# Kernel tuning notes

Measured on AMD Instinct MI355X. Metric: run time of the kernel, lower is better.

The kernel has to match this reference:

```python
import jax, jax.numpy as jnp
import numpy as np

G_DIMS = [30, 30, 24, 18, 18]
G_DOWN = [10, 10, 8, 6, 6]
S_DIM = 10
N_OBJ = 45
N_STREAMS = 5
P_DIM = sum(G_DOWN) * S_DIM          # 400
HID = 20 * S_DIM                     # 200
FREQS = np.array([0.01, 0.7, 0.91, 0.97, 0.99], dtype=np.float32)
DECAY, N_ITERS = 0.8, 5
HEB_LR, HEB_FORGET = 0.5, 0.9999
LOGSIG_RATIO, LOGSIG_OFFSET = 6.0, -2.0
B, T = 256, 8
_G_OFFS = np.concatenate([[0], np.cumsum(G_DIMS)]).astype(int)


def _leaky_clamp(x):
    # f(clamp(x, -1, 1)) with f = leaky_relu (torch default slope 0.01)
    return jax.nn.leaky_relu(jnp.clip(x, -1.0, 1.0))


def _scale_log_sigma(raw, temp=1.0):
    return LOGSIG_OFFSET + temp * jnp.tanh(raw / LOGSIG_RATIO) * LOGSIG_RATIO


def _downsample(g):  # [B, 120] -> [B, 40]; take first g_down dims of each stream
    return jnp.concatenate([g[:, o:o + d] for o, d in zip(_G_OFFS[:-1], G_DOWN)], axis=1)


def setup_inputs() -> dict:
    key = jax.random.key(0)
    ks = jax.random.split(key, 10)
    return {
        "g_seq": jax.random.normal(ks[0], (B, T, sum(G_DIMS)), jnp.float32),
        "x_idx": jax.random.randint(ks[1], (B, T), 0, N_OBJ),
        "W_comp": jax.random.normal(ks[2], (N_OBJ, S_DIM), jnp.float32) * 0.3,
        "W_repeat": jax.random.normal(ks[3], (P_DIM, sum(G_DOWN)), jnp.float32) * 0.2,
        "W_tile": jax.random.normal(ks[4], (P_DIM, N_STREAMS * S_DIM), jnp.float32) * 0.2,
        "W_tile0": jax.random.normal(ks[5], (G_DOWN[0] * S_DIM, S_DIM), jnp.float32) * 0.2,
        "w_x": jnp.ones((), jnp.float32),
        "b_x": jnp.zeros((S_DIM,), jnp.float32),
        "W1": jax.random.normal(ks[6], (S_DIM, HID), jnp.float32) * 0.2,
        "b1": jnp.zeros((HID,), jnp.float32),
        "W2": jax.random.normal(ks[7], (HID, N_OBJ), jnp.float32) * 0.1,
        "b2": jnp.zeros((N_OBJ,), jnp.float32),
        "W_lv1": jax.random.normal(ks[8], (P_DIM, P_DIM), jnp.float32) * 0.05,
        "b_lv1": jnp.zeros((P_DIM,), jnp.float32),
        "W_lv2": jax.random.normal(ks[9], (P_DIM, P_DIM), jnp.float32) * 0.05,
        "b_lv2": jnp.zeros((P_DIM,), jnp.float32),
    }


def _forward(g_seq, x_onehot, W_comp, W_repeat, W_tile, W_tile0, w_x, b_x,
             W1, b1, W2, b2, W_lv1, b_lv1, W_lv2, b_lv2):
    Bn = g_seq.shape[0]
    freqs = jnp.asarray(FREQS, dtype=g_seq.dtype)

    def step(carry, xs):
        M, x_filt = carry            # M: [B,P,P] Hebbian memory; x_filt: [B,5,10]
        g_t, x_t = xs                # g_t: [B,120], x_t: [B,45]
        # sensory compression + per-stream exponential temporal filtering
        x_c = x_t @ W_comp                                          # [B,10]
        x_filt = (1.0 - freqs)[None, :, None] * x_filt + freqs[None, :, None] * x_c[:, None, :]
        x_flat = x_filt.reshape(Bn, N_STREAMS * S_DIM)              # [B,50]
        # fused p-vector formation (_scriptable_fused_form_p)
        g_down = _downsample(g_t)                                   # [B,40]
        g_exp = g_down @ W_repeat.T                                 # [B,400]
        x_exp = x_flat @ W_tile.T                                   # [B,400]
        p_inf = _leaky_clamp(g_exp * x_exp)
        # attractor retrieval seeded from g projected to p-space (_scriptable_transform_g_to_p)
        h = _leaky_clamp(g_exp)
        for _ in range(N_ITERS):                                    # memory_iterations
            h = _leaky_clamp(DECAY * h + jnp.einsum('bij,bj->bi', M, h))
        p_ret = h
        # precision-weighted Gaussian fusion of inference and memory estimates
        lv1 = _scale_log_sigma(p_inf @ W_lv1 + b_lv1)
        lv2 = _scale_log_sigma(p_ret @ W_lv2 + b_lv2)
        inv1, inv2 = jnp.exp(-lv1), jnp.exp(-lv2)
        var_c = 1.0 / (inv1 + inv2)
        p_t = var_c * (p_inf * inv1 + p_ret * inv2)
        # Hebbian update: M <- lambda*M + eta*(p - p_hat)(p + p_hat)^T
        M = HEB_FORGET * M + HEB_LR * jnp.einsum('bi,bj->bij', p_t - p_ret, p_t + p_ret)
        # generative decode from stream-0 slice of p (GenerativeNetwork.forward_decode)
        x_s = w_x * (p_t[:, :G_DOWN[0] * S_DIM] @ W_tile0) + b_x    # [B,10]
        logits = jax.nn.elu(x_s @ W1 + b1) @ W2 + b2                # [B,45]
        return (M, x_filt), logits

    M0 = jnp.zeros((Bn, P_DIM, P_DIM), g_seq.dtype)
    xf0 = jnp.zeros((Bn, N_STREAMS, S_DIM), g_seq.dtype)
    xs = (jnp.swapaxes(g_seq, 0, 1), jnp.swapaxes(x_onehot, 0, 1))
    _, logits = jax.lax.scan(step, (M0, xf0), xs)                   # [T,B,45]
    return jnp.swapaxes(logits, 0, 1)                               # [B,T,45]


def reference(g_seq, x_idx, W_comp, W_repeat, W_tile, W_tile0, w_x, b_x,
              W1, b1, W2, b2, W_lv1, b_lv1, W_lv2, b_lv2):
    x_onehot = jax.nn.one_hot(x_idx, N_OBJ, dtype=g_seq.dtype)
    return _forward(g_seq, x_onehot, W_comp, W_repeat, W_tile, W_tile0, w_x, b_x,
                    W1, b1, W2, b2, W_lv1, b_lv1, W_lv2, b_lv2)
```

## Files before the change

### kernel.cpp

```cpp
#include <hip/hip_runtime.h>

#define kT 8
#define kG 120
#define kP 400
#define kObj 45
#define kS 10
#define kHid 200
#define NL 12
#define NV 24
#define NC (NL + NV)

__device__ __constant__ int c_gmap[40] = {
    0,1,2,3,4,5,6,7,8,9,
    30,31,32,33,34,35,36,37,38,39,
    60,61,62,63,64,65,66,67,
    84,85,86,87,88,89,
    102,103,104,105,106,107};

__device__ __constant__ float c_freq[5] = {0.01f, 0.7f, 0.91f, 0.97f, 0.99f};

__device__ __forceinline__ float leaky_clamp(float x) {
    x = fminf(fmaxf(x, -1.0f), 1.0f);
    return x > 0.0f ? x : 0.01f * x;
}

__global__ __launch_bounds__(512, 1) void tem_kernel(
    const float* __restrict__ g_seq, const int* __restrict__ x_idx,
    const float* __restrict__ W_comp, const float* __restrict__ W_repeat,
    const float* __restrict__ W_tile, const float* __restrict__ W_tile0,
    const float* __restrict__ w_x, const float* __restrict__ b_x,
    const float* __restrict__ W1, const float* __restrict__ b1,
    const float* __restrict__ W2, const float* __restrict__ b2,
    const float* __restrict__ W_lv1, const float* __restrict__ b_lv1,
    const float* __restrict__ W_lv2, const float* __restrict__ b_lv2,
    float* __restrict__ out)
{
    const int b   = blockIdx.x;
    const int tid = threadIdx.x;
    const int dim = tid;
    const bool hasD = (tid < kP);
    const int wid  = tid >> 6;
    const int lane = tid & 63;
    const int g   = tid >> 7;
    const int r   = tid & 127;
    const bool mact = (r < 100);
    const int j0  = g * 100;

    const int soff = ((blockIdx.x >> 3) << 2) & 63;
    const int joff = (((blockIdx.x >> 3) * 16) % kP);

    __shared__ __align__(16) float pT[kP][kT];
    __shared__ __align__(16) float hT[kP][kT];
    __shared__ __align__(16) float lvT[kP][kT];
    __shared__ __align__(16) float xfT[50][kT];
    __shared__ __align__(16) float gdT[40][kT];
    __shared__ __align__(16) float s_wc[4][NL][kP];
    __shared__ float s_h[kP];
    __shared__ float s_pt[kP];
    __shared__ float s_u[kT][kP];
    __shared__ float s_v[kT][kP];
    __shared__ __align__(16) float s_part[4][kP];
    __shared__ float s_red[2][kT][8];
    __shared__ int   s_idx[kT];
    __shared__ float s_xsp[kS][kS];
    __shared__ float s_xs[kS];
    __shared__ float s_hid[kHid];
    __shared__ float s_lp[8][kObj];

    const float blv1 = hasD ? b_lv1[dim] : 0.0f;
    const float blv2 = hasD ? b_lv2[dim] : 0.0f;
    const float wx   = w_x[0];

    if (tid < kT) s_idx[tid] = x_idx[b * kT + tid];
    __syncthreads();

    if (mact) {
        #pragma unroll
        for (int k = 0; k < NL; ++k)
            ((float4*)&s_wc[g][k][0])[r] =
                ((const float4*)(W_lv2 + (j0 + k) * kP))[r];
    }

    if (tid < 40) {
        int gi = c_gmap[tid];
        #pragma unroll
        for (int t = 0; t < kT; ++t)
            gdT[tid][t] = g_seq[(b * kT + t) * kG + gi];
    } else if (tid >= 64 && tid < 114) {
        int rr = tid - 64, d = rr % 10;
        float f = c_freq[rr / 10];
        float xf = 0.0f;
        #pragma unroll
        for (int t = 0; t < kT; ++t) {
            float xc = W_comp[s_idx[t] * kS + d];
            xf = (1.0f - f) * xf + f * xc;
            xfT[rr][t] = xf;
        }
    }
    __syncthreads();

    if (hasD) {
        float ge[kT], xe[kT];
        #pragma unroll
        for (int t = 0; t < kT; ++t) { ge[t] = 0.0f; xe[t] = 0.0f; }
        for (int j = 0; j < 40; ++j) {
            float w = W_repeat[dim * 40 + j];
            float4 gA = *(const float4*)&gdT[j][0];
            float4 gB = *(const float4*)&gdT[j][4];
            ge[0] += w * gA.x; ge[1] += w * gA.y; ge[2] += w * gA.z; ge[3] += w * gA.w;
            ge[4] += w * gB.x; ge[5] += w * gB.y; ge[6] += w * gB.z; ge[7] += w * gB.w;
        }
        for (int j = 0; j < 50; ++j) {
            float w = W_tile[dim * 50 + j];
            float4 xA = *(const float4*)&xfT[j][0];
            float4 xB = *(const float4*)&xfT[j][4];
            xe[0] += w * xA.x; xe[1] += w * xA.y; xe[2] += w * xA.z; xe[3] += w * xA.w;
            xe[4] += w * xB.x; xe[5] += w * xB.y; xe[6] += w * xB.z; xe[7] += w * xB.w;
        }
        float4 pA, pB, hA, hB;
        pA.x = leaky_clamp(ge[0] * xe[0]); pA.y = leaky_clamp(ge[1] * xe[1]);
        pA.z = leaky_clamp(ge[2] * xe[2]); pA.w = leaky_clamp(ge[3] * xe[3]);
        pB.x = leaky_clamp(ge[4] * xe[4]); pB.y = leaky_clamp(ge[5] * xe[5]);
        pB.z = leaky_clamp(ge[6] * xe[6]); pB.w = leaky_clamp(ge[7] * xe[7]);
        hA.x = leaky_clamp(ge[0]); hA.y = leaky_clamp(ge[1]);
        hA.z = leaky_clamp(ge[2]); hA.w = leaky_clamp(ge[3]);
        hB.x = leaky_clamp(ge[4]); hB.y = leaky_clamp(ge[5]);
        hB.z = leaky_clamp(ge[6]); hB.w = leaky_clamp(ge[7]);
        *(float4*)&pT[dim][0] = pA; *(float4*)&pT[dim][4] = pB;
        *(float4*)&hT[dim][0] = hA; *(float4*)&hT[dim][4] = hB;
    }
    __syncthreads();

    if (hasD) {
        float acc[kT];
        #pragma unroll
        for (int t = 0; t < kT; ++t) acc[t] = 0.0f;
        #pragma unroll 4
        for (int j = joff; j < kP; ++j) {
            float w = W_lv1[j * kP + dim];
            float4 pA = *(const float4*)&pT[j][0];
            float4 pB = *(const float4*)&pT[j][4];
            acc[0] += w * pA.x; acc[1] += w * pA.y; acc[2] += w * pA.z; acc[3] += w * pA.w;
            acc[4] += w * pB.x; acc[5] += w * pB.y; acc[6] += w * pB.z; acc[7] += w * pB.w;
        }
        #pragma unroll 4
        for (int j = 0; j < joff; ++j) {
            float w = W_lv1[j * kP + dim];
            float4 pA = *(const float4*)&pT[j][0];
            float4 pB = *(const float4*)&pT[j][4];
            acc[0] += w * pA.x; acc[1] += w * pA.y; acc[2] += w * pA.z; acc[3] += w * pA.w;
            acc[4] += w * pB.x; acc[5] += w * pB.y; acc[6] += w * pB.z; acc[7] += w * pB.w;
        }
        *(float4*)&lvT[dim][0] = make_float4(acc[0], acc[1], acc[2], acc[3]);
        *(float4*)&lvT[dim][4] = make_float4(acc[4], acc[5], acc[6], acc[7]);
    }
    __syncthreads();

    float4 wreg[NV];
    if (mact) {
        #pragma unroll
        for (int k = 0; k < NV; ++k)
            wreg[k] = ((const float4*)(W_lv2 + (j0 + NL + k) * kP))[r];
    }

    int par = 0;
    for (int t = 0; t < kT; ++t) {
        float h = hasD ? hT[dim][t] : 0.0f;
        if (t == 0) {
            #pragma unroll
            for (int it = 0; it < 5; ++it) h = leaky_clamp(0.8f * h);
        } else {
            for (int it = 0; it < 5; ++it) {
                for (int s = 0; s < t; ++s) {
                    float p = hasD ? s_v[s][dim] * h : 0.0f;
                    #pragma unroll
                    for (int off = 32; off; off >>= 1) p += __shfl_down(p, off, 64);
                    if (lane == 0) s_red[par][s][wid] = p;
                }
                __syncthreads();
                if (hasD) {
                    float mh = 0.0f;
                    float c = 0.5f;
                    for (int s = t - 1; s >= 0; --s) {
                        float d = 0.0f;
                        #pragma unroll
                        for (int w = 0; w < 8; ++w) d += s_red[par][s][w];
                        mh += c * d * s_u[s][dim];
                        c *= 0.9999f;
                    }
                    h = leaky_clamp(0.8f * h + mh);
                }
                par ^= 1;
            }
        }
        if (hasD) s_h[dim] = h;
        __syncthreads();

        if (mact) {
            float4 a0{0,0,0,0}, a1{0,0,0,0}, a2{0,0,0,0}, a3{0,0,0,0};
            #pragma unroll
            for (int k = 0; k < NL; k += 4) {
                int j = j0 + k;
                float4 w0 = ((const float4*)&s_wc[g][k+0][0])[r];
                float4 w1v = ((const float4*)&s_wc[g][k+1][0])[r];
                float4 w2v = ((const float4*)&s_wc[g][k+2][0])[r];
                float4 w3 = ((const float4*)&s_wc[g][k+3][0])[r];
                float v0 = s_h[j+0], v1 = s_h[j+1], v2 = s_h[j+2], v3 = s_h[j+3];
                a0.x += w0.x * v0; a0.y += w0.y * v0; a0.z += w0.z * v0; a0.w += w0.w * v0;
                a1.x += w1v.x * v1; a1.y += w1v.y * v1; a1.z += w1v.z * v1; a1.w += w1v.w * v1;
                a2.x += w2v.x * v2; a2.y += w2v.y * v2; a2.z += w2v.z * v2; a2.w += w2v.w * v2;
                a3.x += w3.x * v3; a3.y += w3.y * v3; a3.z += w3.z * v3; a3.w += w3.w * v3;
            }
            #pragma unroll
            for (int k = 0; k < NV; k += 4) {
                int j = j0 + NL + k;
                float v0 = s_h[j+0], v1 = s_h[j+1], v2 = s_h[j+2], v3 = s_h[j+3];
                a0.x += wreg[k].x * v0; a0.y += wreg[k].y * v0; a0.z += wreg[k].z * v0; a0.w += wreg[k].w * v0;
                a1.x += wreg[k+1].x * v1; a1.y += wreg[k+1].y * v1; a1.z += wreg[k+1].z * v1; a1.w += wreg[k+1].w * v1;
                a2.x += wreg[k+2].x * v2; a2.y += wreg[k+2].y * v2; a2.z += wreg[k+2].z * v2; a2.w += wreg[k+2].w * v2;
                a3.x += wreg[k+3].x * v3; a3.y += wreg[k+3].y * v3; a3.z += wreg[k+3].z * v3; a3.w += wreg[k+3].w * v3;
            }
            #pragma unroll 2
            for (int jj = 0; jj < 64; jj += 4) {
                int j = j0 + NC + ((jj + soff) & 63);
                float4 w0 = ((const float4*)(W_lv2 + (j+0) * kP))[r];
                float4 w1v = ((const float4*)(W_lv2 + (j+1) * kP))[r];
                float4 w2v = ((const float4*)(W_lv2 + (j+2) * kP))[r];
                float4 w3 = ((const float4*)(W_lv2 + (j+3) * kP))[r];
                float v0 = s_h[j+0], v1 = s_h[j+1], v2 = s_h[j+2], v3 = s_h[j+3];
                a0.x += w0.x * v0; a0.y += w0.y * v0; a0.z += w0.z * v0; a0.w += w0.w * v0;
                a1.x += w1v.x * v1; a1.y += w1v.y * v1; a1.z += w1v.z * v1; a1.w += w1v.w * v1;
                a2.x += w2v.x * v2; a2.y += w2v.y * v2; a2.z += w2v.z * v2; a2.w += w2v.w * v2;
                a3.x += w3.x * v3; a3.y += w3.y * v3; a3.z += w3.z * v3; a3.w += w3.w * v3;
            }
            float4 tot;
            tot.x = (a0.x + a1.x) + (a2.x + a3.x);
            tot.y = (a0.y + a1.y) + (a2.y + a3.y);
            tot.z = (a0.z + a1.z) + (a2.z + a3.z);
            tot.w = (a0.w + a1.w) + (a2.w + a3.w);
            ((float4*)&s_part[g][0])[r] = tot;
        }
        __syncthreads();

        if (hasD) {
            float lv2raw = (s_part[0][dim] + s_part[1][dim])
                         + (s_part[2][dim] + s_part[3][dim]) + blv2;
            float lv1raw = lvT[dim][t] + blv1;
            float l1 = -2.0f + 6.0f * tanhf(lv1raw * (1.0f / 6.0f));
            float l2 = -2.0f + 6.0f * tanhf(lv2raw * (1.0f / 6.0f));
            float i1v = expf(-l1), i2v = expf(-l2);
            float pinf = pT[dim][t];
            float p = (pinf * i1v + h * i2v) / (i1v + i2v);
            s_pt[dim] = p;
            s_u[t][dim] = p - h;
            s_v[t][dim] = p + h;
        }
        __syncthreads();

        if (tid < 100) {
            int d = tid % 10, c = tid / 10;
            float acc = 0.0f;
            #pragma unroll
            for (int jj = 0; jj < 10; ++jj) {
                int j = c * 10 + jj;
                acc += s_pt[j] * W_tile0[j * kS + d];
            }
            s_xsp[c][d] = acc;
        }
        __syncthreads();
        if (tid < kS) {
            float acc = 0.0f;
            #pragma unroll
            for (int c = 0; c < 10; ++c) acc += s_xsp[c][tid];
            s_xs[tid] = wx * acc + b_x[tid];
        }
        __syncthreads();
        if (tid < kHid) {
            float acc = b1[tid];
            #pragma unroll
            for (int d = 0; d < kS; ++d)
                acc += s_xs[d] * W1[d * kHid + tid];
            s_hid[tid] = acc > 0.0f ? acc : (expf(acc) - 1.0f);
        }
        __syncthreads();
        if (tid < 360) {
            int o = tid % kObj, c = tid / kObj;
            float acc = 0.0f;
            #pragma unroll
            for (int hh = 0; hh < 25; ++hh) {
                int hI = c * 25 + hh;
                acc += s_hid[hI] * W2[hI * kObj + o];
            }
            s_lp[c][o] = acc;
        }
        __syncthreads();
        if (tid < kObj) {
            float acc = b2[tid];
            #pragma unroll
            for (int c = 0; c < 8; ++c) acc += s_lp[c][tid];
            out[(b * kT + t) * kObj + tid] = acc;
        }
        __syncthreads();
    }
}

extern "C" void kernel_launch(void* const* d_in, const int* in_sizes, int n_in,
                              void* d_out, int out_size, void* d_ws, size_t ws_size,
                              hipStream_t stream) {
    const float* g_seq   = (const float*)d_in[0];
    const int*   x_idx   = (const int*)d_in[1];
    const float* W_comp  = (const float*)d_in[2];
    const float* W_repeat= (const float*)d_in[3];
    const float* W_tile  = (const float*)d_in[4];
    const float* W_tile0 = (const float*)d_in[5];
    const float* w_x     = (const float*)d_in[6];
    const float* b_x     = (const float*)d_in[7];
    const float* W1      = (const float*)d_in[8];
    const float* b1      = (const float*)d_in[9];
    const float* W2      = (const float*)d_in[10];
    const float* b2      = (const float*)d_in[11];
    const float* W_lv1   = (const float*)d_in[12];
    const float* b_lv1   = (const float*)d_in[13];
    const float* W_lv2   = (const float*)d_in[14];
    const float* b_lv2   = (const float*)d_in[15];
    float* out = (float*)d_out;

    const int Bn = in_sizes[0] / (kT * kG);
    tem_kernel<<<dim3(Bn), dim3(512), 0, stream>>>(
        g_seq, x_idx, W_comp, W_repeat, W_tile, W_tile0, w_x, b_x,
        W1, b1, W2, b2, W_lv1, b_lv1, W_lv2, b_lv2, out);
}
```

Before: 210.6 us.

## Batch decoder MLP over all timesteps after the recurrence and stagger weight slices

Moves the per-timestep generative decode (W_tile0, W1, W2 chain with five barriers per step) out of the serial time loop and runs it once for all 8 timesteps after the loop. p is rebuilt from the stored u and v. This removes about 40 block-wide barriers and lets more threads work in parallel on the decode. It also rotates which W_lv2 quarter each group loads per block phase, changes the soff/joff staggering and the unroll shape of the global-load loop, all to spread memory traffic across blocks. Rebuilding p from the sum and difference adds a small rounding difference.

```diff
diff --git a/kernel.cpp b/kernel.cpp
--- a/kernel.cpp
+++ b/kernel.cpp
@@ -44,10 +44,12 @@
     const int g   = tid >> 7;
     const int r   = tid & 127;
     const bool mact = (r < 100);
-    const int j0  = g * 100;
-
-    const int soff = ((blockIdx.x >> 3) << 2) & 63;
-    const int joff = (((blockIdx.x >> 3) * 16) % kP);
+
+    const int phase = blockIdx.x >> 3;
+    const int q   = (g + phase) & 3;
+    const int qj0 = q * 100;
+    const int soff = (phase * 2) & 63;
+    const int joff = (phase * 13) % kP;
 
     __shared__ __align__(16) float pT[kP][kT];
     __shared__ __align__(16) float hT[kP][kT];
@@ -56,16 +58,11 @@
     __shared__ __align__(16) float gdT[40][kT];
     __shared__ __align__(16) float s_wc[4][NL][kP];
     __shared__ float s_h[kP];
-    __shared__ float s_pt[kP];
     __shared__ float s_u[kT][kP];
     __shared__ float s_v[kT][kP];
     __shared__ __align__(16) float s_part[4][kP];
     __shared__ float s_red[2][kT][8];
     __shared__ int   s_idx[kT];
-    __shared__ float s_xsp[kS][kS];
-    __shared__ float s_xs[kS];
-    __shared__ float s_hid[kHid];
-    __shared__ float s_lp[8][kObj];
 
     const float blv1 = hasD ? b_lv1[dim] : 0.0f;
     const float blv2 = hasD ? b_lv2[dim] : 0.0f;
@@ -78,7 +75,7 @@
         #pragma unroll
         for (int k = 0; k < NL; ++k)
             ((float4*)&s_wc[g][k][0])[r] =
-                ((const float4*)(W_lv2 + (j0 + k) * kP))[r];
+                ((const float4*)(W_lv2 + (qj0 + k) * kP))[r];
     }
 
     if (tid < 40) {
@@ -160,7 +157,7 @@
     if (mact) {
         #pragma unroll
         for (int k = 0; k < NV; ++k)
-            wreg[k] = ((const float4*)(W_lv2 + (j0 + NL + k) * kP))[r];
+            wreg[k] = ((const float4*)(W_lv2 + (qj0 + NL + k) * kP))[r];
     }
 
     int par = 0;
@@ -200,7 +197,7 @@
             float4 a0{0,0,0,0}, a1{0,0,0,0}, a2{0,0,0,0}, a3{0,0,0,0};
             #pragma unroll
             for (int k = 0; k < NL; k += 4) {
-                int j = j0 + k;
+                int j = qj0 + k;
                 float4 w0 = ((const float4*)&s_wc[g][k+0][0])[r];
                 float4 w1v = ((const float4*)&s_wc[g][k+1][0])[r];
                 float4 w2v = ((const float4*)&s_wc[g][k+2][0])[r];
@@ -213,25 +210,21 @@
             }
             #pragma unroll
             for (int k = 0; k < NV; k += 4) {
-                int j = j0 + NL + k;
+                int j = qj0 + NL + k;
                 float v0 = s_h[j+0], v1 = s_h[j+1], v2 = s_h[j+2], v3 = s_h[j+3];
                 a0.x += wreg[k].x * v0; a0.y += wreg[k].y * v0; a0.z += wreg[k].z * v0; a0.w += wreg[k].w * v0;
                 a1.x += wreg[k+1].x * v1; a1.y += wreg[k+1].y * v1; a1.z += wreg[k+1].z * v1; a1.w += wreg[k+1].w * v1;
                 a2.x += wreg[k+2].x * v2; a2.y += wreg[k+2].y * v2; a2.z += wreg[k+2].z * v2; a2.w += wreg[k+2].w * v2;
                 a3.x += wreg[k+3].x * v3; a3.y += wreg[k+3].y * v3; a3.z += wreg[k+3].z * v3; a3.w += wreg[k+3].w * v3;
             }
-            #pragma unroll 2
-            for (int jj = 0; jj < 64; jj += 4) {
-                int j = j0 + NC + ((jj + soff) & 63);
+            #pragma unroll 4
+            for (int jj = 0; jj < 64; jj += 2) {
+                int j = qj0 + NC + ((jj + soff) & 63);
                 float4 w0 = ((const float4*)(W_lv2 + (j+0) * kP))[r];
                 float4 w1v = ((const float4*)(W_lv2 + (j+1) * kP))[r];
-                float4 w2v = ((const float4*)(W_lv2 + (j+2) * kP))[r];
-                float4 w3 = ((const float4*)(W_lv2 + (j+3) * kP))[r];
-                float v0 = s_h[j+0], v1 = s_h[j+1], v2 = s_h[j+2], v3 = s_h[j+3];
+                float v0 = s_h[j+0], v1 = s_h[j+1];
                 a0.x += w0.x * v0; a0.y += w0.y * v0; a0.z += w0.z * v0; a0.w += w0.w * v0;
                 a1.x += w1v.x * v1; a1.y += w1v.y * v1; a1.z += w1v.z * v1; a1.w += w1v.w * v1;
-                a2.x += w2v.x * v2; a2.y += w2v.y * v2; a2.z += w2v.z * v2; a2.w += w2v.w * v2;
-                a3.x += w3.x * v3; a3.y += w3.y * v3; a3.z += w3.z * v3; a3.w += w3.w * v3;
             }
             float4 tot;
             tot.x = (a0.x + a1.x) + (a2.x + a3.x);
@@ -251,56 +244,58 @@
             float i1v = expf(-l1), i2v = expf(-l2);
             float pinf = pT[dim][t];
             float p = (pinf * i1v + h * i2v) / (i1v + i2v);
-            s_pt[dim] = p;
             s_u[t][dim] = p - h;
             s_v[t][dim] = p + h;
         }
-        __syncthreads();
-
-        if (tid < 100) {
-            int d = tid % 10, c = tid / 10;
-            float acc = 0.0f;
-            #pragma unroll
-            for (int jj = 0; jj < 10; ++jj) {
-                int j = c * 10 + jj;
-                acc += s_pt[j] * W_tile0[j * kS + d];
-            }
-            s_xsp[c][d] = acc;
-        }
-        __syncthreads();
-        if (tid < kS) {
-            float acc = 0.0f;
-            #pragma unroll
-            for (int c = 0; c < 10; ++c) acc += s_xsp[c][tid];
-            s_xs[tid] = wx * acc + b_x[tid];
-        }
-        __syncthreads();
-        if (tid < kHid) {
-            float acc = b1[tid];
-            #pragma unroll
-            for (int d = 0; d < kS; ++d)
-                acc += s_xs[d] * W1[d * kHid + tid];
-            s_hid[tid] = acc > 0.0f ? acc : (expf(acc) - 1.0f);
-        }
-        __syncthreads();
-        if (tid < 360) {
-            int o = tid % kObj, c = tid / kObj;
-            float acc = 0.0f;
-            #pragma unroll
-            for (int hh = 0; hh < 25; ++hh) {
-                int hI = c * 25 + hh;
-                acc += s_hid[hI] * W2[hI * kObj + o];
-            }
-            s_lp[c][o] = acc;
-        }
-        __syncthreads();
-        if (tid < kObj) {
-            float acc = b2[tid];
-            #pragma unroll
-            for (int c = 0; c < 8; ++c) acc += s_lp[c][tid];
-            out[(b * kT + t) * kObj + tid] = acc;
-        }
-        __syncthreads();
+    }
+    __syncthreads();
+
+    float* dsc  = &hT[0][0];
+    float* dhid = &lvT[0][0];
+
+    if (tid < 480) {
+        int t = tid / 60, rem = tid % 60;
+        int d = rem / 6, k = rem % 6;
+        int jlo = k * 17, jhi = (jlo + 17 > 100) ? 100 : jlo + 17;
+        float acc = 0.0f;
+        for (int j = jlo; j < jhi; ++j) {
+            float pj = 0.5f * (s_u[t][j] + s_v[t][j]);
+            acc += pj * W_tile0[j * kS + d];
+        }
+        dsc[(t * 10 + d) * 6 + k] = acc;
+    }
+    __syncthreads();
+    if (tid < 80) {
+        int t = tid / 10, d = tid % 10;
+        float acc = 0.0f;
+        #pragma unroll
+        for (int k = 0; k < 6; ++k) acc += dsc[(t * 10 + d) * 6 + k];
+        dsc[1000 + t * 10 + d] = wx * acc + b_x[d];
+    }
+    __syncthreads();
+    for (int idx = tid; idx < kT * kHid; idx += 512) {
+        int t = idx / kHid, hh = idx - t * kHid;
+        float acc = b1[hh];
+        #pragma unroll
+        for (int d = 0; d < kS; ++d)
+            acc += dsc[1000 + t * 10 + d] * W1[d * kHid + hh];
+        dhid[t * kHid + hh] = acc > 0.0f ? acc : (expf(acc) - 1.0f);
+    }
+    __syncthreads();
+    for (int idx = tid; idx < 720; idx += 512) {
+        int t = idx / 90, rem = idx - t * 90;
+        int half = rem / kObj, o = rem - half * kObj;
+        int h0 = half * 100;
+        float acc = 0.0f;
+        for (int hh = h0; hh < h0 + 100; ++hh)
+            acc += dhid[t * kHid + hh] * W2[hh * kObj + o];
+        dsc[2000 + idx] = acc;
+    }
+    __syncthreads();
+    if (tid < 360) {
+        int t = tid / kObj, o = tid - t * kObj;
+        out[(b * kT + t) * kObj + o] =
+            b2[o] + dsc[2000 + t * 90 + o] + dsc[2000 + t * 90 + kObj + o];
     }
 }
 
```

After: 206.0 us, median of 2. 2.2% less time.
